# Performance work log

Hardware: AMD Instinct MI355X
Metric: run time of the kernel (lower is better)

Reference implementation:

```python
import jax, jax.numpy as jnp
import numpy as np


def setup_inputs() -> dict:
    key = jax.random.key(0)
    k1, k2 = jax.random.split(key)
    B, N, M = 4, 8192, 8192
    xyz1 = jax.random.normal(k1, (B, N, 3), dtype=jnp.float32)
    xyz2 = jax.random.normal(k2, (B, M, 3), dtype=jnp.float32)
    return {"xyz1": xyz1, "xyz2": xyz2}


def _chamfer(xyz1, xyz2):
    sq1 = jnp.sum(xyz1 * xyz1, axis=-1)  # [B, N]
    sq2 = jnp.sum(xyz2 * xyz2, axis=-1)  # [B, M]
    inner = jnp.einsum("bnc,bmc->bnm", xyz1, xyz2)  # [B, N, M]
    d = sq1[:, :, None] + sq2[:, None, :] - 2.0 * inner
    dist1 = jnp.min(d, axis=2)  # [B, N] nearest in xyz2 for each xyz1 point
    dist2 = jnp.min(d, axis=1)  # [B, M] nearest in xyz1 for each xyz2 point
    return dist1, dist2


def reference(xyz1, xyz2):
    return _chamfer(xyz1, xyz2)
```

## Files before the change

kernel.cpp:

```cpp
#include <hip/hip_runtime.h>

typedef _Float16 half8 __attribute__((ext_vector_type(8)));
typedef float f32x16 __attribute__((ext_vector_type(16)));

#define NQ 4

__device__ __forceinline__ float min3f(float a, float b, float c) {
    float d;
    asm("v_min3_f32 %0, %1, %2, %3" : "=v"(d) : "v"(a), "v"(b), "v"(c));
    return d;
}

__global__ void cd_prep(const float* __restrict__ xyz1,
                        const float* __restrict__ xyz2,
                        _Float16* __restrict__ frag) {
    int tid  = blockIdx.x * 256 + threadIdx.x;
    int aidx = tid >> 14;
    int rem  = tid & 16383;
    int g = rem >> 6, l = rem & 63;
    int dir = aidx >> 2, b = aidx & 3;
    const float* src = (dir ? xyz1 : xyz2) + (size_t)b * 8192 * 3;
    int t = g * 32 + (l & 31);
    float x = src[t*3+0], y = src[t*3+1], z = src[t*3+2];
    float sq = __builtin_fmaf(x, x, __builtin_fmaf(y, y, z * z));
    _Float16 xh = (_Float16)x, yh = (_Float16)y, zh = (_Float16)z;
    _Float16 xl = (_Float16)(x - (float)xh);
    _Float16 yl = (_Float16)(y - (float)yh);
    _Float16 zl = (_Float16)(z - (float)zh);
    _Float16 sh = (_Float16)sq;
    _Float16 sl = (_Float16)(sq - (float)sh);
    const _Float16 one = (_Float16)1.0f, zero = (_Float16)0.0f;
    half8 f;
    if ((l >> 5) == 0) {
        f[0]=xh; f[1]=xh; f[2]=xl; f[3]=yh; f[4]=yh; f[5]=yl; f[6]=zh; f[7]=zh;
    } else {
        f[0]=zl; f[1]=sh; f[2]=sl; f[3]=one; f[4]=one; f[5]=zero; f[6]=zero; f[7]=zero;
    }
    ((half8*)frag)[(size_t)aidx * 16384 + g * 64 + l] = f;
}

#define FOLD(Dv, bj)                                   \
    bj = min3f(Dv[0],  Dv[1],  bj);                    \
    bj = min3f(Dv[2],  Dv[3],  bj);                    \
    bj = min3f(Dv[4],  Dv[5],  bj);                    \
    bj = min3f(Dv[6],  Dv[7],  bj);                    \
    bj = min3f(Dv[8],  Dv[9],  bj);                    \
    bj = min3f(Dv[10], Dv[11], bj);                    \
    bj = min3f(Dv[12], Dv[13], bj);                    \
    bj = min3f(Dv[14], Dv[15], bj);

__global__ void __launch_bounds__(256) cd_main(
        const float* __restrict__ xyz1, const float* __restrict__ xyz2,
        const _Float16* __restrict__ frag, float* __restrict__ out) {
    __shared__ float red[4][128];
    const int qt  = blockIdx.x;
    const int bd  = blockIdx.y;
    const int dir = bd >> 2, b = bd & 3;
    const int l = threadIdx.x & 63, w = threadIdx.x >> 6;
    const int h = l >> 5;
    const float* q = (dir ? xyz2 : xyz1) + (size_t)b * 8192 * 3;
    const int qbase = qt * 128;

    half8 Bf[NQ];
    const _Float16 one = (_Float16)1.0f, zero = (_Float16)0.0f;
    #pragma unroll
    for (int j = 0; j < NQ; ++j) {
        int qi = qbase + j * 32 + (l & 31);
        float px = q[qi*3+0], py = q[qi*3+1], pz = q[qi*3+2];
        float mx = -2.f * px, my = -2.f * py, mz = -2.f * pz;
        float sq = __builtin_fmaf(px, px, __builtin_fmaf(py, py, pz * pz));
        _Float16 mxh = (_Float16)mx, mxl = (_Float16)(mx - (float)mxh);
        _Float16 myh = (_Float16)my, myl = (_Float16)(my - (float)myh);
        _Float16 mzh = (_Float16)mz, mzl = (_Float16)(mz - (float)mzh);
        _Float16 sh  = (_Float16)sq, sl  = (_Float16)(sq - (float)sh);
        half8 f;
        if (h == 0) { f[0]=mxh; f[1]=mxl; f[2]=mxh; f[3]=myh; f[4]=myl; f[5]=myh; f[6]=mzh; f[7]=mzl; }
        else        { f[0]=mzh; f[1]=one; f[2]=one; f[3]=sh; f[4]=sl; f[5]=zero; f[6]=zero; f[7]=zero; }
        Bf[j] = f;
    }

    f32x16 Z;
    #pragma unroll
    for (int i = 0; i < 16; ++i) Z[i] = 0.f;

    float best[NQ];
    #pragma unroll
    for (int j = 0; j < NQ; ++j) best[j] = 3.0e38f;

    const half8* Ap = ((const half8*)frag) + (size_t)bd * 16384 + w * 4096 + l;

    half8 a = Ap[0];
    #pragma unroll 2
    for (int g = 0; g < 63; ++g) {
        half8 an = Ap[(size_t)(g + 1) * 64];
        #pragma unroll
        for (int j = 0; j < NQ; ++j) {
            f32x16 D = __builtin_amdgcn_mfma_f32_32x32x16_f16(a, Bf[j], Z, 0, 0, 0);
            FOLD(D, best[j]);
        }
        a = an;
    }
    #pragma unroll
    for (int j = 0; j < NQ; ++j) {
        f32x16 D = __builtin_amdgcn_mfma_f32_32x32x16_f16(a, Bf[j], Z, 0, 0, 0);
        FOLD(D, best[j]);
    }

    #pragma unroll
    for (int j = 0; j < NQ; ++j) {
        float o = __shfl_xor(best[j], 32, 64);
        best[j] = fminf(best[j], o);
    }
    if (l < 32) {
        #pragma unroll
        for (int j = 0; j < NQ; ++j) red[w][j * 32 + l] = best[j];
    }
    __syncthreads();
    if (threadIdx.x < 128) {
        int t = threadIdx.x;
        float m = fminf(fminf(red[0][t], red[1][t]), fminf(red[2][t], red[3][t]));
        out[(size_t)dir * 32768 + (size_t)b * 8192 + qbase + t] = m;
    }
}

extern "C" void kernel_launch(void* const* d_in, const int* in_sizes, int n_in,
                              void* d_out, int out_size, void* d_ws, size_t ws_size,
                              hipStream_t stream) {
    const float* xyz1 = (const float*)d_in[0];
    const float* xyz2 = (const float*)d_in[1];
    _Float16* frag = (_Float16*)d_ws;

    cd_prep<<<512, 256, 0, stream>>>(xyz1, xyz2, frag);

    dim3 grid(64, 8);
    cd_main<<<grid, 256, 0, stream>>>(xyz1, xyz2, frag, (float*)d_out);
}
```

Measured before the change: 34.76 us.

## Split target points across blocks and merge partial minima with atomicMin

Adds a grid dimension of four splits over the target points, so each block scans only a quarter of the fragment data. Grid size goes from 512 to 2048 blocks, which should keep more wavefronts resident to hide MFMA and load latency. Partial minima are merged with an unsigned-integer atomicMin on the float bits, after a memset that fills the output with a large value. The loop is now fully unrolled with a double-buffered prefetch. This adds a memset launch and atomic traffic, and the integer-ordered min is wrong for any slightly negative distance produced by rounding.

```diff
diff --git a/kernel.cpp b/kernel.cpp
--- a/kernel.cpp
+++ b/kernel.cpp
@@ -4,6 +4,8 @@
 typedef float f32x16 __attribute__((ext_vector_type(16)));
 
 #define NQ 4
+#define TS 4
+#define GPW 16
 
 __device__ __forceinline__ float min3f(float a, float b, float c) {
     float d;
@@ -51,10 +53,11 @@
 
 __global__ void __launch_bounds__(256) cd_main(
         const float* __restrict__ xyz1, const float* __restrict__ xyz2,
-        const _Float16* __restrict__ frag, float* __restrict__ out) {
+        const _Float16* __restrict__ frag, unsigned int* __restrict__ out) {
     __shared__ float red[4][128];
-    const int qt  = blockIdx.x;
-    const int bd  = blockIdx.y;
+    const int ts  = blockIdx.x;
+    const int qt  = blockIdx.y;
+    const int bd  = blockIdx.z;
     const int dir = bd >> 2, b = bd & 3;
     const int l = threadIdx.x & 63, w = threadIdx.x >> 6;
     const int h = l >> 5;
@@ -87,23 +90,23 @@
     #pragma unroll
     for (int j = 0; j < NQ; ++j) best[j] = 3.0e38f;
 
-    const half8* Ap = ((const half8*)frag) + (size_t)bd * 16384 + w * 4096 + l;
+    const half8* Ap = ((const half8*)frag) + (size_t)bd * 16384
+                      + ((size_t)ts * 64 + (size_t)w * GPW) * 64 + l;
 
-    half8 a = Ap[0];
-    #pragma unroll 2
-    for (int g = 0; g < 63; ++g) {
-        half8 an = Ap[(size_t)(g + 1) * 64];
+    half8 buf0 = Ap[0];
+    half8 buf1 = Ap[64];
+    #pragma unroll
+    for (int g = 0; g < GPW; ++g) {
+        half8 a = (g & 1) ? buf1 : buf0;
+        if (g + 2 < GPW) {
+            if (g & 1) buf1 = Ap[(size_t)(g + 2) * 64];
+            else       buf0 = Ap[(size_t)(g + 2) * 64];
+        }
         #pragma unroll
         for (int j = 0; j < NQ; ++j) {
             f32x16 D = __builtin_amdgcn_mfma_f32_32x32x16_f16(a, Bf[j], Z, 0, 0, 0);
             FOLD(D, best[j]);
         }
-        a = an;
-    }
-    #pragma unroll
-    for (int j = 0; j < NQ; ++j) {
-        f32x16 D = __builtin_amdgcn_mfma_f32_32x32x16_f16(a, Bf[j], Z, 0, 0, 0);
-        FOLD(D, best[j]);
     }
 
     #pragma unroll
@@ -119,7 +122,8 @@
     if (threadIdx.x < 128) {
         int t = threadIdx.x;
         float m = fminf(fminf(red[0][t], red[1][t]), fminf(red[2][t], red[3][t]));
-        out[(size_t)dir * 32768 + (size_t)b * 8192 + qbase + t] = m;
+        atomicMin(out + (size_t)dir * 32768 + (size_t)b * 8192 + qbase + t,
+                  __float_as_uint(m));
     }
 }
 
@@ -130,8 +134,10 @@
     const float* xyz2 = (const float*)d_in[1];
     _Float16* frag = (_Float16*)d_ws;
 
+    hipMemsetAsync(d_out, 0x7F, (size_t)out_size * sizeof(float), stream);
+
     cd_prep<<<512, 256, 0, stream>>>(xyz1, xyz2, frag);
 
-    dim3 grid(64, 8);
-    cd_main<<<grid, 256, 0, stream>>>(xyz1, xyz2, frag, (float*)d_out);
+    dim3 grid(TS, 64, 8);
+    cd_main<<<grid, 256, 0, stream>>>(xyz1, xyz2, frag, (unsigned int*)d_out);
 }
```

Result: slower. 36.75 us (+5.7%).
